# Optimization experiments

Measured on AMD Instinct MI355X. Metric: run time of the kernel, lower is better.

The kernel has to match this reference:

```python
import jax, jax.numpy as jnp
import numpy as np

NUM_LAYERS = 2
D = 1024
DIN = 2048
N_STATE = 16
K = 4
EPS = 1e-5


def layer_norm(x, w, b):
    m = jnp.mean(x, axis=-1, keepdims=True)
    v = jnp.mean(jnp.square(x - m), axis=-1, keepdims=True)
    return (x - m) * jax.lax.rsqrt(v + EPS) * w + b


def selective_ssm(x, A_log, Wdt, b_dt, WB, WC, D_skip):
    # x: [B, L, DIN]; diagonal selective SSM (Mamba-style)
    A = -jnp.exp(A_log)                      # [DIN, N]
    dt = jax.nn.softplus(x @ Wdt + b_dt)     # [B, L, DIN]
    Bm = x @ WB                              # [B, L, N]
    Cm = x @ WC                              # [B, L, N]

    def step(h, inp):
        x_t, dt_t, B_t, C_t = inp            # [B,DIN],[B,DIN],[B,N],[B,N]
        dA = jnp.exp(dt_t[..., None] * A)    # [B, DIN, N]
        h = h * dA + (dt_t * x_t)[..., None] * B_t[:, None, :]
        y = jnp.einsum('bdn,bn->bd', h, C_t)
        return h, y

    xs = (x.transpose(1, 0, 2), dt.transpose(1, 0, 2),
          Bm.transpose(1, 0, 2), Cm.transpose(1, 0, 2))
    h0 = jnp.zeros((x.shape[0], x.shape[2], N_STATE), x.dtype)
    h_last, ys = jax.lax.scan(step, h0, xs)
    y = ys.transpose(1, 0, 2) + x * D_skip
    return y, h_last


def causal_dwconv(x, w, b):
    # x: [B, L, DIN]; w: [K, DIN] depthwise causal conv
    xp = jnp.pad(x, ((0, 0), (K - 1, 0), (0, 0)))
    out = jax.lax.conv_general_dilated(
        xp, w[:, None, :], (1,), 'VALID',
        dimension_numbers=('NWC', 'WIO', 'NWC'),
        feature_group_count=x.shape[-1])
    return out + b


def setup_inputs() -> dict:
    key = jax.random.key(0)
    ks = jax.random.split(key, 12)
    s = 0.02
    B, L = 2, 2048
    return {
        'x': jax.random.normal(ks[0], (B, L, D), jnp.float32),
        'pos_emb': jax.random.normal(ks[1], (L, D), jnp.float32) * s,
        'norm_w': jnp.ones((NUM_LAYERS, D), jnp.float32),
        'norm_b': jnp.zeros((NUM_LAYERS, D), jnp.float32),
        'Win': jax.random.normal(ks[2], (NUM_LAYERS, D, DIN), jnp.float32) * s,
        'b_in': jnp.zeros((NUM_LAYERS, DIN), jnp.float32),
        'A_log': jax.random.uniform(ks[3], (NUM_LAYERS, DIN, N_STATE), jnp.float32),
        'Wdt': jax.random.normal(ks[4], (NUM_LAYERS, DIN, DIN), jnp.float32) * s,
        'b_dt': jax.random.normal(ks[5], (NUM_LAYERS, DIN), jnp.float32) - 4.0,
        'WB': jax.random.normal(ks[6], (NUM_LAYERS, DIN, N_STATE), jnp.float32) * s,
        'WC': jax.random.normal(ks[7], (NUM_LAYERS, DIN, N_STATE), jnp.float32) * s,
        'D_skip': jnp.ones((NUM_LAYERS, DIN), jnp.float32),
        'conv_w': jax.random.normal(ks[8], (NUM_LAYERS, K, DIN), jnp.float32) * s,
        'conv_b': jnp.zeros((NUM_LAYERS, DIN), jnp.float32),
        'Wout': jax.random.normal(ks[9], (NUM_LAYERS, DIN, D), jnp.float32) * s,
        'b_out': jnp.zeros((NUM_LAYERS, D), jnp.float32),
        'fnorm_w': jnp.ones((D,), jnp.float32),
        'fnorm_b': jnp.zeros((D,), jnp.float32),
    }


def reference(x, pos_emb, norm_w, norm_b, Win, b_in, A_log, Wdt, b_dt, WB, WC,
              D_skip, conv_w, conv_b, Wout, b_out, fnorm_w, fnorm_b):
    L = x.shape[1]
    x = x + pos_emb[:L]
    for i in range(NUM_LAYERS):
        res = x
        h = layer_norm(x, norm_w[i], norm_b[i])
        h = h @ Win[i] + b_in[i]                       # [B, L, DIN]
        y_ssm, _ = selective_ssm(h, A_log[i], Wdt[i], b_dt[i], WB[i], WC[i], D_skip[i])
        y_conv = jax.nn.silu(causal_dwconv(h, conv_w[i], conv_b[i]))
        g = y_ssm * jax.nn.sigmoid(y_conv)             # gating
        x = g @ Wout[i] + b_out[i] + res               # dropout is identity (eval)
    return layer_norm(x, fnorm_w, fnorm_b)
```

## Files before the change

### kernel.cpp

```cpp
#include <hip/hip_runtime.h>
#include <cstdint>
#include <cstddef>

#define D_MODEL 1024
#define DIN     2048
#define NSTATE  16
#define LSEQ    2048
#define NBATCH  2
#define NROWS   (NBATCH*LSEQ)
#define NCOL    (DIN + 128)
#define CCH     64
#define TC      (LSEQ/CCH)

typedef float  f32x4  __attribute__((ext_vector_type(4)));
typedef short  bf16x8 __attribute__((ext_vector_type(8)));
typedef unsigned short us8 __attribute__((ext_vector_type(8)));

__device__ __forceinline__ unsigned short f2bf(float f) {
  union { float f; unsigned u; } c; c.f = f;
  unsigned x = c.u + 0x7fffu + ((c.u >> 16) & 1u);
  return (unsigned short)(x >> 16);
}
__device__ __forceinline__ float bf2f(unsigned short u) {
  union { unsigned u; float f; } c; c.u = (unsigned)u << 16; return c.f;
}
__device__ __forceinline__ float sigmoidf_(float x) {
  return __builtin_amdgcn_rcpf(1.f + __expf(-x));
}
__device__ __forceinline__ float softplusf_(float x) {
  return fmaxf(x, 0.f) + __logf(1.f + __expf(-fabsf(x)));
}

__device__ __forceinline__ void gll16(const void* g, void* l) {
  __builtin_amdgcn_global_load_lds(
      (const __attribute__((address_space(1))) void*)g,
      (__attribute__((address_space(3))) void*)l, 16, 0, 0);
}

__global__ __launch_bounds__(256) void ln_kernel(const float* __restrict__ Xin,
    const float* __restrict__ pos, const unsigned short* __restrict__ P, int nP,
    const float* __restrict__ bex, const float* __restrict__ w,
    const float* __restrict__ b, unsigned short* __restrict__ outB,
    float* __restrict__ outF, float* __restrict__ Xw) {
  const int row = blockIdx.x, t = threadIdx.x;
  float4 v = *(const float4*)(Xin + (size_t)row * D_MODEL + t * 4);
  if (pos) {
    const float4 p = *(const float4*)(pos + (size_t)(row & (LSEQ - 1)) * D_MODEL + t * 4);
    v.x += p.x; v.y += p.y; v.z += p.z; v.w += p.w;
  }
  if (P) {
    const size_t MN = (size_t)NROWS * D_MODEL;
    const size_t e = (size_t)row * D_MODEL + t * 4;
    float a0 = 0.f, a1 = 0.f, a2 = 0.f, a3 = 0.f;
#pragma unroll 4
    for (int k = 0; k < nP; k++) {
      const ushort4 u = *(const ushort4*)(P + k * MN + e);
      a0 += bf2f(u.x); a1 += bf2f(u.y); a2 += bf2f(u.z); a3 += bf2f(u.w);
    }
    const float4 be = *(const float4*)(bex + t * 4);
    v.x += a0 + be.x; v.y += a1 + be.y; v.z += a2 + be.z; v.w += a3 + be.w;
  }
  if (Xw) *(float4*)(Xw + (size_t)row * D_MODEL + t * 4) = v;
  float s  = v.x + v.y + v.z + v.w;
  float s2 = v.x * v.x + v.y * v.y + v.z * v.z + v.w * v.w;
#pragma unroll
  for (int o = 1; o < 64; o <<= 1) { s += __shfl_xor(s, o, 64); s2 += __shfl_xor(s2, o, 64); }
  __shared__ float ps[8];
  int wv = t >> 6;
  if ((t & 63) == 0) { ps[wv] = s; ps[wv + 4] = s2; }
  __syncthreads();
  s  = ps[0] + ps[1] + ps[2] + ps[3];
  s2 = ps[4] + ps[5] + ps[6] + ps[7];
  float mean = s * (1.f / D_MODEL);
  float var  = s2 * (1.f / D_MODEL) - mean * mean;
  float rs   = rsqrtf(var + 1e-5f);
  const float4 wv4 = *(const float4*)(w + t * 4);
  const float4 bv4 = *(const float4*)(b + t * 4);
  float o0 = (v.x - mean) * rs * wv4.x + bv4.x;
  float o1 = (v.y - mean) * rs * wv4.y + bv4.y;
  float o2 = (v.z - mean) * rs * wv4.z + bv4.z;
  float o3 = (v.w - mean) * rs * wv4.w + bv4.w;
  if (outB) {
    ushort4 o; o.x = f2bf(o0); o.y = f2bf(o1); o.z = f2bf(o2); o.w = f2bf(o3);
    *(ushort4*)(outB + (size_t)row * D_MODEL + t * 4) = o;
  } else {
    float4 o; o.x = o0; o.y = o1; o.z = o2; o.w = o3;
    *(float4*)(outF + (size_t)row * D_MODEL + t * 4) = o;
  }
}

__global__ __launch_bounds__(256) void tcvt_kernel(const float* __restrict__ in0,
    unsigned short* __restrict__ out0, int K_, int N_,
    size_t inLS, size_t outLS) {
  const float* in = in0 + (size_t)blockIdx.z * inLS;
  unsigned short* out = out0 + (size_t)blockIdx.z * outLS;
  __shared__ float tile[64][68];
  int n0 = blockIdx.x * 64, k0 = blockIdx.y * 64;
  int t = threadIdx.x;
  int r = t >> 4, cc = (t & 15) * 4;
#pragma unroll
  for (int j = 0; j < 4; j++) {
    const float4 v = *(const float4*)(in + (size_t)(k0 + r + j * 16) * N_ + n0 + cc);
    tile[r + j * 16][cc + 0] = v.x; tile[r + j * 16][cc + 1] = v.y;
    tile[r + j * 16][cc + 2] = v.z; tile[r + j * 16][cc + 3] = v.w;
  }
  __syncthreads();
  int nr = t >> 2, kc = (t & 3) * 16;
  unsigned u[8];
#pragma unroll
  for (int i = 0; i < 8; i++) {
    unsigned lo = f2bf(tile[kc + 2 * i][nr]);
    unsigned hi = f2bf(tile[kc + 2 * i + 1][nr]);
    u[i] = lo | (hi << 16);
  }
  uint4* dst = (uint4*)(out + (size_t)(n0 + nr) * K_ + k0 + kc);
  uint4 w0; w0.x = u[0]; w0.y = u[1]; w0.z = u[2]; w0.w = u[3];
  uint4 w1; w1.x = u[4]; w1.y = u[5]; w1.z = u[6]; w1.w = u[7];
  dst[0] = w0; dst[1] = w1;
}

__global__ __launch_bounds__(256) void wprep_kernel(const float* __restrict__ WB0,
    const float* __restrict__ WC0, const float* __restrict__ b_dt0,
    unsigned short* __restrict__ Wt0, float* __restrict__ bias20) {
  const int L = blockIdx.y;
  const float* WB = WB0 + (size_t)L * DIN * NSTATE;
  const float* WC = WC0 + (size_t)L * DIN * NSTATE;
  const float* b_dt = b_dt0 + (size_t)L * DIN;
  unsigned short* Wt = Wt0 + (size_t)L * NCOL * DIN;
  float* bias2 = bias20 + (size_t)L * NCOL;
  int id = blockIdx.x * 256 + threadIdx.x;
  if (id < 65536) {
    int k = id & (DIN - 1);
    int n2 = id >> 11;
    float v = (n2 < NSTATE) ? WB[(size_t)k * NSTATE + n2]
                            : WC[(size_t)k * NSTATE + (n2 - NSTATE)];
    Wt[(size_t)(DIN + n2) * DIN + k] = f2bf(v);
  } else if (id < 90112) {
    int z = id - 65536;
    uint4 zz; zz.x = zz.y = zz.z = zz.w = 0u;
    *(uint4*)(Wt + (size_t)2080 * DIN + (size_t)z * 8) = zz;
  } else if (id < 90112 + NCOL) {
    int i = id - 90112;
    bias2[i] = (i < DIN) ? b_dt[i] : 0.f;
  }
}

__global__ __launch_bounds__(256) void gemm_kernel(
    const unsigned short* __restrict__ A, const unsigned short* __restrict__ Bt,
    const float* __restrict__ bias, unsigned short* __restrict__ outP,
    int M, int N, int Kfull, int kLen) {
  __shared__ unsigned short smem[6 * 128 * 32];
  unsigned short* sA = smem;
  unsigned short* sB = smem + 3 * 4096;
  const int t = threadIdx.x;
  const int lane = t & 63, wave = t >> 6;
  const int wr = wave >> 1, wc = wave & 1;

  const int gx = gridDim.x, gy = gridDim.y;
  const int orig = (blockIdx.z * gy + blockIdx.y) * gx + blockIdx.x;
  const int nwg = gx * gy * gridDim.z;
  const int q = nwg >> 3, r = nwg & 7;
  const int xcd = orig & 7, pp = orig >> 3;
  const int wgid = (xcd < r) ? (xcd * (q + 1) + pp)
                             : (r * (q + 1) + (xcd - r) * q + pp);
  const int nt = wgid % gx;
  const int mt = (wgid / gx) % gy;
  const int ks = wgid / (gx * gy);
  const int m0 = mt * 128, n0 = nt * 128;

  const int ar = t >> 2;
  const int acs = (((t & 3) ^ ((ar >> 1) & 3)) << 3);
  const int wseg = wave * 16 * 32;
  const int lr = lane & 15;
  const int swA = (((lane >> 4) ^ ((lr >> 1) & 3)) << 3);

  f32x4 acc[4][4];
#pragma unroll
  for (int m = 0; m < 4; m++)
#pragma unroll
    for (int n = 0; n < 4; n++) acc[m][n] = (f32x4)0.f;

  const int kBeg = ks * kLen;
  const int NT = kLen >> 5;

  auto STAGE = [&](int bi, int k0) {
    gll16(A  + (size_t)(m0 + ar) * Kfull + k0 + acs,      &sA[bi * 4096 + wseg]);
    gll16(A  + (size_t)(m0 + 64 + ar) * Kfull + k0 + acs, &sA[bi * 4096 + 64 * 32 + wseg]);
    gll16(Bt + (size_t)(n0 + ar) * Kfull + k0 + acs,      &sB[bi * 4096 + wseg]);
    gll16(Bt + (size_t)(n0 + 64 + ar) * Kfull + k0 + acs, &sB[bi * 4096 + 64 * 32 + wseg]);
  };
  auto COMPUTE = [&](int bi) {
    bf16x8 af[4], bg[4];
#pragma unroll
    for (int m = 0; m < 4; m++)
      af[m] = *(const bf16x8*)(&sA[bi * 4096 + (wr * 64 + m * 16 + lr) * 32 + swA]);
#pragma unroll
    for (int n = 0; n < 4; n++)
      bg[n] = *(const bf16x8*)(&sB[bi * 4096 + (wc * 64 + n * 16 + lr) * 32 + swA]);
#pragma unroll
    for (int m = 0; m < 4; m++)
#pragma unroll
      for (int n = 0; n < 4; n++)
        acc[m][n] = __builtin_amdgcn_mfma_f32_16x16x32_bf16(af[m], bg[n], acc[m][n], 0, 0, 0);
  };

  STAGE(0, kBeg); STAGE(1, kBeg + 32);
  for (int tt = 0; tt < NT - 1; ++tt) {
    asm volatile("s_waitcnt vmcnt(4)" ::: "memory");
    __builtin_amdgcn_s_barrier();
    if (tt + 2 < NT) STAGE((tt + 2) % 3, kBeg + ((tt + 2) << 5));
    COMPUTE(tt % 3);
  }
  asm volatile("s_waitcnt vmcnt(0)" ::: "memory");
  __builtin_amdgcn_s_barrier();
  COMPUTE((NT - 1) % 3);

  __syncthreads();
  unsigned short* sC = smem + wave * 4096;
  const int lq = lane >> 4;
#pragma unroll
  for (int m = 0; m < 4; m++)
#pragma unroll
    for (int n = 0; n < 4; n++) {
      const int lcol = n * 16 + lr;
      const float bv = (bias && ks == 0) ? bias[n0 + wc * 64 + lcol] : 0.f;
#pragma unroll
      for (int j = 0; j < 4; j++) {
        const int lrow = m * 16 + lq * 4 + j;
        const int sc = lcol ^ (((lrow >> 2) & 3) << 4);
        sC[lrow * 64 + sc] = f2bf(acc[m][n][j] + bv);
      }
    }
  unsigned short* out = outP + (size_t)ks * M * N;
  const int rowbase = m0 + wr * 64, colbase = n0 + wc * 64;
  const int rr = lane >> 3, ch = lane & 7;
#pragma unroll
  for (int i = 0; i < 8; i++) {
    const int row = i * 8 + rr;
    const int sb = (ch * 16) ^ (((row >> 2) & 3) << 5);
    us8 v = *(const us8*)((const char*)sC + row * 128 + sb);
    *(us8*)(out + (size_t)(rowbase + row) * N + colbase + ch * 8) = v;
  }
}

__global__ __launch_bounds__(256) void hfin_kernel(const unsigned short* __restrict__ P,
    const float* __restrict__ bias, unsigned short* __restrict__ Hbf) {
  const size_t e = ((size_t)blockIdx.x * 256 + threadIdx.x) * 4;
  const int col = (int)(e & (DIN - 1));
  const ushort4 u0 = *(const ushort4*)(P + e);
  const ushort4 u1 = *(const ushort4*)(P + (size_t)NROWS * DIN + e);
  const float4 b = *(const float4*)(bias + col);
  ushort4 o;
  o.x = f2bf(bf2f(u0.x) + bf2f(u1.x) + b.x);
  o.y = f2bf(bf2f(u0.y) + bf2f(u1.y) + b.y);
  o.z = f2bf(bf2f(u0.z) + bf2f(u1.z) + b.z);
  o.w = f2bf(bf2f(u0.w) + bf2f(u1.w) + b.w);
  *(ushort4*)(Hbf + e) = o;
}

__global__ __launch_bounds__(256) void scan1_kernel(
    const unsigned short* __restrict__ DTP, const unsigned short* __restrict__ Hbf,
    const float* __restrict__ A_log, float* __restrict__ Hc, float* __restrict__ Pc) {
  const unsigned short* DT1 = DTP + (size_t)NROWS * NCOL;
  const int tid = threadIdx.x;
  const int d0 = blockIdx.x * 256, d = d0 + tid;
  const int b = blockIdx.y, c = blockIdx.z;
  __shared__ unsigned short ssp[TC][256];
  __shared__ unsigned short sxx[TC][256];
  __shared__ float sBC[TC][32];
  const size_t base = (size_t)b * LSEQ + c * TC;
#pragma unroll
  for (int it = 0; it < TC * 32 / 256; ++it) {
    int idx = it * 256 + tid;
    int tt = idx >> 5, cc = (idx & 31) * 8;
    us8 a = *(const us8*)(DTP + (base + tt) * NCOL + d0 + cc);
    us8 bb = *(const us8*)(DT1 + (base + tt) * NCOL + d0 + cc);
    us8 o;
#pragma unroll
    for (int j = 0; j < 8; j++) o[j] = f2bf(softplusf_(bf2f(a[j]) + bf2f(bb[j])));
    *(us8*)&ssp[tt][cc] = o;
    *(us8*)&sxx[tt][cc] = *(const us8*)(Hbf + (base + tt) * DIN + d0 + cc);
  }
  if (tid < TC * 4) {
    int tt = tid >> 2, cc = (tid & 3) * 8;
    us8 v0 = *(const us8*)(DTP + (base + tt) * NCOL + DIN + cc);
    us8 v1 = *(const us8*)(DT1 + (base + tt) * NCOL + DIN + cc);
#pragma unroll
    for (int j = 0; j < 8; j++) sBC[tt][cc + j] = bf2f(v0[j]) + bf2f(v1[j]);
  }
  float a2[16], h[16];
#pragma unroll
  for (int n = 0; n < 16; n++) {
    a2[n] = -__expf(A_log[(size_t)d * NSTATE + n]);
    h[n] = 0.f;
  }
  __syncthreads();
  float S = 0.f;
  for (int tt = 0; tt < TC; ++tt) {
    float sp = bf2f(ssp[tt][tid]);
    float x  = bf2f(sxx[tt][tid]);
    S += sp;
    float sx = sp * x;
#pragma unroll
    for (int n = 0; n < 16; n++)
      h[n] = fmaf(h[n], __expf(sp * a2[n]), sx * sBC[tt][n]);
  }
  const size_t chain = ((size_t)c * (NBATCH * DIN) + (size_t)b * DIN + d) * 16;
#pragma unroll
  for (int n = 0; n < 16; n++) {
    Hc[chain + n] = h[n];
    Pc[chain + n] = __expf(S * a2[n]);
  }
}

__global__ __launch_bounds__(256) void scomb_kernel(float* __restrict__ Hc,
    const float* __restrict__ Pc) {
  const size_t id = (size_t)blockIdx.x * 256 + threadIdx.x;
  const size_t stride = (size_t)NBATCH * DIN * NSTATE;
  float h = 0.f;
  for (int c = 0; c < CCH; c++) {
    size_t o = (size_t)c * stride + id;
    float hl = Hc[o], p = Pc[o];
    Hc[o] = h;
    h = fmaf(p, h, hl);
  }
}

__global__ __launch_bounds__(256) void scan2g_kernel(
    const unsigned short* __restrict__ DTP, const unsigned short* __restrict__ Hbf,
    const float* __restrict__ A_log, const float* __restrict__ Hinit,
    const float* __restrict__ cw, const float* __restrict__ cb,
    const float* __restrict__ dsk, unsigned short* __restrict__ G) {
  const unsigned short* DT1 = DTP + (size_t)NROWS * NCOL;
  const int tid = threadIdx.x;
  const int d0 = blockIdx.x * 256, d = d0 + tid;
  const int b = blockIdx.y, c = blockIdx.z;
  __shared__ unsigned short ssp[TC][256];
  __shared__ unsigned short sxx[TC][256];
  __shared__ float sBC[TC][32];
  const size_t base = (size_t)b * LSEQ + c * TC;
#pragma unroll
  for (int it = 0; it < TC * 32 / 256; ++it) {
    int idx = it * 256 + tid;
    int tt = idx >> 5, cc = (idx & 31) * 8;
    us8 a = *(const us8*)(DTP + (base + tt) * NCOL + d0 + cc);
    us8 bb = *(const us8*)(DT1 + (base + tt) * NCOL + d0 + cc);
    us8 o;
#pragma unroll
    for (int j = 0; j < 8; j++) o[j] = f2bf(softplusf_(bf2f(a[j]) + bf2f(bb[j])));
    *(us8*)&ssp[tt][cc] = o;
    *(us8*)&sxx[tt][cc] = *(const us8*)(Hbf + (base + tt) * DIN + d0 + cc);
  }
  if (tid < TC * 4) {
    int tt = tid >> 2, cc = (tid & 3) * 8;
    us8 v0 = *(const us8*)(DTP + (base + tt) * NCOL + DIN + cc);
    us8 v1 = *(const us8*)(DT1 + (base + tt) * NCOL + DIN + cc);
#pragma unroll
    for (int j = 0; j < 8; j++) sBC[tt][cc + j] = bf2f(v0[j]) + bf2f(v1[j]);
  }
  const size_t chain = ((size_t)c * (NBATCH * DIN) + (size_t)b * DIN + d) * 16;
  float a2[16], h[16];
#pragma unroll
  for (int n = 0; n < 16; n++) {
    a2[n] = -__expf(A_log[(size_t)d * NSTATE + n]);
    h[n] = Hinit[chain + n];
  }
  const float w0 = cw[d], w1 = cw[DIN + d], w2 = cw[2 * DIN + d], w3 = cw[3 * DIN + d];
  const float cbv = cb[d], dsv = dsk[d];
  const int t0 = c * TC;
  float xm1 = (t0 >= 1) ? bf2f(Hbf[(base - 1) * DIN + d]) : 0.f;
  float xm2 = (t0 >= 2) ? bf2f(Hbf[(base - 2) * DIN + d]) : 0.f;
  float xm3 = (t0 >= 3) ? bf2f(Hbf[(base - 3) * DIN + d]) : 0.f;
  __syncthreads();
  for (int tt = 0; tt < TC; ++tt) {
    float sp = bf2f(ssp[tt][tid]);
    float x  = bf2f(sxx[tt][tid]);
    float sx = sp * x;
    float y0 = 0.f, y1 = 0.f, y2 = 0.f, y3 = 0.f;
#pragma unroll
    for (int n = 0; n < 16; n += 4) {
      h[n]     = fmaf(h[n],     __expf(sp * a2[n]),     sx * sBC[tt][n]);
      h[n + 1] = fmaf(h[n + 1], __expf(sp * a2[n + 1]), sx * sBC[tt][n + 1]);
      h[n + 2] = fmaf(h[n + 2], __expf(sp * a2[n + 2]), sx * sBC[tt][n + 2]);
      h[n + 3] = fmaf(h[n + 3], __expf(sp * a2[n + 3]), sx * sBC[tt][n + 3]);
      y0 = fmaf(h[n],     sBC[tt][16 + n],     y0);
      y1 = fmaf(h[n + 1], sBC[tt][16 + n + 1], y1);
      y2 = fmaf(h[n + 2], sBC[tt][16 + n + 2], y2);
      y3 = fmaf(h[n + 3], sBC[tt][16 + n + 3], y3);
    }
    float y = (y0 + y1) + (y2 + y3);
    float a = cbv + w0 * xm3 + w1 * xm2 + w2 * xm1 + w3 * x;
    float sl = a * sigmoidf_(a);
    float g = (y + x * dsv) * sigmoidf_(sl);
    G[(base + tt) * DIN + d] = f2bf(g);
    xm3 = xm2; xm2 = xm1; xm1 = x;
  }
}

extern "C" void kernel_launch(void* const* d_in, const int* in_sizes, int n_in,
                              void* d_out, int out_size, void* d_ws, size_t ws_size,
                              hipStream_t stream) {
  const float* x_in   = (const float*)d_in[0];
  const float* pos    = (const float*)d_in[1];
  const float* norm_w = (const float*)d_in[2];
  const float* norm_b = (const float*)d_in[3];
  const float* Win    = (const float*)d_in[4];
  const float* b_in   = (const float*)d_in[5];
  const float* A_log  = (const float*)d_in[6];
  const float* Wdt    = (const float*)d_in[7];
  const float* b_dt   = (const float*)d_in[8];
  const float* WB     = (const float*)d_in[9];
  const float* WC     = (const float*)d_in[10];
  const float* Dsk    = (const float*)d_in[11];
  const float* conv_w = (const float*)d_in[12];
  const float* conv_b = (const float*)d_in[13];
  const float* Wout   = (const float*)d_in[14];
  const float* b_out  = (const float*)d_in[15];
  const float* fnw    = (const float*)d_in[16];
  const float* fnb    = (const float*)d_in[17];

  uint8_t* ws = (uint8_t*)d_ws;
  constexpr size_t OFF_X     = 0;
  constexpr size_t OFF_HBF   = 16777216;
  constexpr size_t OFF_DT    = 33554432;
  constexpr size_t OFF_XG    = 69206016;
  constexpr size_t OFF_HC    = 85983232;
  constexpr size_t OFF_PC    = 102760448;
  constexpr size_t OFF_WINT  = 119537664;
  constexpr size_t OFF_WDT   = 127926272;
  constexpr size_t OFF_WOUT  = 145752064;
  constexpr size_t OFF_BIAS2 = 154140672;
  constexpr size_t WS_NEEDED = 154158080;
  if (ws_size < WS_NEEDED) return;

  float* X             = (float*)(ws + OFF_X);
  unsigned short* Hbf  = (unsigned short*)(ws + OFF_HBF);
  unsigned short* DTP  = (unsigned short*)(ws + OFF_DT);
  unsigned short* Xn   = (unsigned short*)(ws + OFF_XG);
  unsigned short* Gb   = (unsigned short*)(ws + OFF_XG);
  float* Hc            = (float*)(ws + OFF_HC);
  float* Pc            = (float*)(ws + OFF_PC);
  unsigned short* WinT   = (unsigned short*)(ws + OFF_WINT);
  unsigned short* WdtBCT = (unsigned short*)(ws + OFF_WDT);
  unsigned short* WoutT  = (unsigned short*)(ws + OFF_WOUT);
  float* bias2         = (float*)(ws + OFF_BIAS2);

  tcvt_kernel<<<dim3(32, 16, 2), 256, 0, stream>>>(
      Win, WinT, 1024, 2048, (size_t)D_MODEL * DIN, (size_t)DIN * D_MODEL);
  tcvt_kernel<<<dim3(32, 32, 2), 256, 0, stream>>>(
      Wdt, WdtBCT, 2048, 2048, (size_t)DIN * DIN, (size_t)NCOL * DIN);
  tcvt_kernel<<<dim3(16, 32, 2), 256, 0, stream>>>(
      Wout, WoutT, 2048, 1024, (size_t)DIN * D_MODEL, (size_t)D_MODEL * DIN);
  wprep_kernel<<<dim3(361, 2), 256, 0, stream>>>(WB, WC, b_dt, WdtBCT, bias2);

  for (int i = 0; i < 2; i++) {
    unsigned short* WinT_i   = WinT + (size_t)i * DIN * D_MODEL;
    unsigned short* WdtBCT_i = WdtBCT + (size_t)i * NCOL * DIN;
    unsigned short* WoutT_i  = WoutT + (size_t)i * D_MODEL * DIN;
    float* bias2_i           = bias2 + (size_t)i * NCOL;

    if (i == 0)
      ln_kernel<<<4096, 256, 0, stream>>>(x_in, pos, nullptr, 0, nullptr,
                                          norm_w, norm_b, Xn, nullptr, X);
    else
      ln_kernel<<<4096, 256, 0, stream>>>(X, nullptr, DTP, 4, b_out,
                                          norm_w + D_MODEL, norm_b + D_MODEL,
                                          Xn, nullptr, X);
    gemm_kernel<<<dim3(16, 32, 2), 256, 0, stream>>>(
        Xn, WinT_i, nullptr, DTP, NROWS, DIN, D_MODEL, 512);
    hfin_kernel<<<8192, 256, 0, stream>>>(DTP, b_in + (size_t)i * DIN, Hbf);
    gemm_kernel<<<dim3(17, 32, 2), 256, 0, stream>>>(
        Hbf, WdtBCT_i, bias2_i, DTP, NROWS, NCOL, DIN, 1024);
    scan1_kernel<<<dim3(DIN / 256, NBATCH, CCH), 256, 0, stream>>>(
        DTP, Hbf, A_log + (size_t)i * DIN * NSTATE, Hc, Pc);
    scomb_kernel<<<(NBATCH * DIN * NSTATE) / 256, 256, 0, stream>>>(Hc, Pc);
    scan2g_kernel<<<dim3(DIN / 256, NBATCH, CCH), 256, 0, stream>>>(
        DTP, Hbf, A_log + (size_t)i * DIN * NSTATE, Hc,
        conv_w + (size_t)i * 4 * DIN, conv_b + (size_t)i * DIN,
        Dsk + (size_t)i * DIN, Gb);
    gemm_kernel<<<dim3(8, 32, 4), 256, 0, stream>>>(
        Gb, WoutT_i, nullptr, DTP, NROWS, D_MODEL, DIN, 512);
  }

  ln_kernel<<<4096, 256, 0, stream>>>(X, nullptr, DTP, 4, b_out + D_MODEL,
                                      fnw, fnb, nullptr, (float*)d_out, nullptr);
}
```

Measured before the change: 465.9 us.

## Drop split-K on Win/Wdt GEMMs, fuse bias and softplus into epilogue

The Win and Wdt/B/C GEMMs no longer use split-K. Bias, and softplus for the dt columns, are now applied in the GEMM epilogue. This removes the hfin reduction kernel and the per-scan-kernel summing of two partial buffers and softplus recomputation. The Wout GEMM split-K drops from 4 to 2, so the layer-norm kernels reduce fewer partials. The cost is fewer workgroups per GEMM (512 and 544 tiles, 512 for Wout) and longer K loops per tile, which may lower occupancy across the CUs.

```diff
diff --git a/kernel.cpp b/kernel.cpp
--- a/kernel.cpp
+++ b/kernel.cpp
@@ -52,7 +52,7 @@
     const size_t MN = (size_t)NROWS * D_MODEL;
     const size_t e = (size_t)row * D_MODEL + t * 4;
     float a0 = 0.f, a1 = 0.f, a2 = 0.f, a3 = 0.f;
-#pragma unroll 4
+#pragma unroll 2
     for (int k = 0; k < nP; k++) {
       const ushort4 u = *(const ushort4*)(P + k * MN + e);
       a0 += bf2f(u.x); a1 += bf2f(u.y); a2 += bf2f(u.z); a3 += bf2f(u.w);
@@ -148,7 +148,7 @@
 __global__ __launch_bounds__(256) void gemm_kernel(
     const unsigned short* __restrict__ A, const unsigned short* __restrict__ Bt,
     const float* __restrict__ bias, unsigned short* __restrict__ outP,
-    int M, int N, int Kfull, int kLen) {
+    int M, int N, int Kfull, int kLen, int spCols) {
   __shared__ unsigned short smem[6 * 128 * 32];
   unsigned short* sA = smem;
   unsigned short* sB = smem + 3 * 4096;
@@ -223,12 +223,16 @@
 #pragma unroll
     for (int n = 0; n < 4; n++) {
       const int lcol = n * 16 + lr;
-      const float bv = (bias && ks == 0) ? bias[n0 + wc * 64 + lcol] : 0.f;
+      const int col = n0 + wc * 64 + lcol;
+      const float bv = (bias && ks == 0) ? bias[col] : 0.f;
+      const bool sp = col < spCols;
 #pragma unroll
       for (int j = 0; j < 4; j++) {
         const int lrow = m * 16 + lq * 4 + j;
         const int sc = lcol ^ (((lrow >> 2) & 3) << 4);
-        sC[lrow * 64 + sc] = f2bf(acc[m][n][j] + bv);
+        float v = acc[m][n][j] + bv;
+        if (sp) v = softplusf_(v);
+        sC[lrow * 64 + sc] = f2bf(v);
       }
     }
   unsigned short* out = outP + (size_t)ks * M * N;
@@ -243,25 +247,9 @@
   }
 }
 
-__global__ __launch_bounds__(256) void hfin_kernel(const unsigned short* __restrict__ P,
-    const float* __restrict__ bias, unsigned short* __restrict__ Hbf) {
-  const size_t e = ((size_t)blockIdx.x * 256 + threadIdx.x) * 4;
-  const int col = (int)(e & (DIN - 1));
-  const ushort4 u0 = *(const ushort4*)(P + e);
-  const ushort4 u1 = *(const ushort4*)(P + (size_t)NROWS * DIN + e);
-  const float4 b = *(const float4*)(bias + col);
-  ushort4 o;
-  o.x = f2bf(bf2f(u0.x) + bf2f(u1.x) + b.x);
-  o.y = f2bf(bf2f(u0.y) + bf2f(u1.y) + b.y);
-  o.z = f2bf(bf2f(u0.z) + bf2f(u1.z) + b.z);
-  o.w = f2bf(bf2f(u0.w) + bf2f(u1.w) + b.w);
-  *(ushort4*)(Hbf + e) = o;
-}
-
 __global__ __launch_bounds__(256) void scan1_kernel(
-    const unsigned short* __restrict__ DTP, const unsigned short* __restrict__ Hbf,
+    const unsigned short* __restrict__ DTF, const unsigned short* __restrict__ Hbf,
     const float* __restrict__ A_log, float* __restrict__ Hc, float* __restrict__ Pc) {
-  const unsigned short* DT1 = DTP + (size_t)NROWS * NCOL;
   const int tid = threadIdx.x;
   const int d0 = blockIdx.x * 256, d = d0 + tid;
   const int b = blockIdx.y, c = blockIdx.z;
@@ -273,20 +261,14 @@
   for (int it = 0; it < TC * 32 / 256; ++it) {
     int idx = it * 256 + tid;
     int tt = idx >> 5, cc = (idx & 31) * 8;
-    us8 a = *(const us8*)(DTP + (base + tt) * NCOL + d0 + cc);
-    us8 bb = *(const us8*)(DT1 + (base + tt) * NCOL + d0 + cc);
-    us8 o;
-#pragma unroll
-    for (int j = 0; j < 8; j++) o[j] = f2bf(softplusf_(bf2f(a[j]) + bf2f(bb[j])));
-    *(us8*)&ssp[tt][cc] = o;
+    *(us8*)&ssp[tt][cc] = *(const us8*)(DTF + (base + tt) * NCOL + d0 + cc);
     *(us8*)&sxx[tt][cc] = *(const us8*)(Hbf + (base + tt) * DIN + d0 + cc);
   }
   if (tid < TC * 4) {
     int tt = tid >> 2, cc = (tid & 3) * 8;
-    us8 v0 = *(const us8*)(DTP + (base + tt) * NCOL + DIN + cc);
-    us8 v1 = *(const us8*)(DT1 + (base + tt) * NCOL + DIN + cc);
-#pragma unroll
-    for (int j = 0; j < 8; j++) sBC[tt][cc + j] = bf2f(v0[j]) + bf2f(v1[j]);
+    us8 v = *(const us8*)(DTF + (base + tt) * NCOL + DIN + cc);
+#pragma unroll
+    for (int j = 0; j < 8; j++) sBC[tt][cc + j] = bf2f(v[j]);
   }
   float a2[16], h[16];
 #pragma unroll
@@ -327,11 +309,10 @@
 }
 
 __global__ __launch_bounds__(256) void scan2g_kernel(
-    const unsigned short* __restrict__ DTP, const unsigned short* __restrict__ Hbf,
+    const unsigned short* __restrict__ DTF, const unsigned short* __restrict__ Hbf,
     const float* __restrict__ A_log, const float* __restrict__ Hinit,
     const float* __restrict__ cw, const float* __restrict__ cb,
     const float* __restrict__ dsk, unsigned short* __restrict__ G) {
-  const unsigned short* DT1 = DTP + (size_t)NROWS * NCOL;
   const int tid = threadIdx.x;
   const int d0 = blockIdx.x * 256, d = d0 + tid;
   const int b = blockIdx.y, c = blockIdx.z;
@@ -343,20 +324,14 @@
   for (int it = 0; it < TC * 32 / 256; ++it) {
     int idx = it * 256 + tid;
     int tt = idx >> 5, cc = (idx & 31) * 8;
-    us8 a = *(const us8*)(DTP + (base + tt) * NCOL + d0 + cc);
-    us8 bb = *(const us8*)(DT1 + (base + tt) * NCOL + d0 + cc);
-    us8 o;
-#pragma unroll
-    for (int j = 0; j < 8; j++) o[j] = f2bf(softplusf_(bf2f(a[j]) + bf2f(bb[j])));
-    *(us8*)&ssp[tt][cc] = o;
+    *(us8*)&ssp[tt][cc] = *(const us8*)(DTF + (base + tt) * NCOL + d0 + cc);
     *(us8*)&sxx[tt][cc] = *(const us8*)(Hbf + (base + tt) * DIN + d0 + cc);
   }
   if (tid < TC * 4) {
     int tt = tid >> 2, cc = (tid & 3) * 8;
-    us8 v0 = *(const us8*)(DTP + (base + tt) * NCOL + DIN + cc);
-    us8 v1 = *(const us8*)(DT1 + (base + tt) * NCOL + DIN + cc);
-#pragma unroll
-    for (int j = 0; j < 8; j++) sBC[tt][cc + j] = bf2f(v0[j]) + bf2f(v1[j]);
+    us8 v = *(const us8*)(DTF + (base + tt) * NCOL + DIN + cc);
+#pragma unroll
+    for (int j = 0; j < 8; j++) sBC[tt][cc + j] = bf2f(v[j]);
   }
   const size_t chain = ((size_t)c * (NBATCH * DIN) + (size_t)b * DIN + d) * 16;
   float a2[16], h[16];
@@ -435,7 +410,8 @@
 
   float* X             = (float*)(ws + OFF_X);
   unsigned short* Hbf  = (unsigned short*)(ws + OFF_HBF);
-  unsigned short* DTP  = (unsigned short*)(ws + OFF_DT);
+  unsigned short* DTF  = (unsigned short*)(ws + OFF_DT);
+  unsigned short* WoutP= (unsigned short*)(ws + OFF_DT);
   unsigned short* Xn   = (unsigned short*)(ws + OFF_XG);
   unsigned short* Gb   = (unsigned short*)(ws + OFF_XG);
   float* Hc            = (float*)(ws + OFF_HC);
@@ -463,25 +439,24 @@
       ln_kernel<<<4096, 256, 0, stream>>>(x_in, pos, nullptr, 0, nullptr,
                                           norm_w, norm_b, Xn, nullptr, X);
     else
-      ln_kernel<<<4096, 256, 0, stream>>>(X, nullptr, DTP, 4, b_out,
+      ln_kernel<<<4096, 256, 0, stream>>>(X, nullptr, WoutP, 2, b_out,
                                           norm_w + D_MODEL, norm_b + D_MODEL,
                                           Xn, nullptr, X);
-    gemm_kernel<<<dim3(16, 32, 2), 256, 0, stream>>>(
-        Xn, WinT_i, nullptr, DTP, NROWS, DIN, D_MODEL, 512);
-    hfin_kernel<<<8192, 256, 0, stream>>>(DTP, b_in + (size_t)i * DIN, Hbf);
-    gemm_kernel<<<dim3(17, 32, 2), 256, 0, stream>>>(
-        Hbf, WdtBCT_i, bias2_i, DTP, NROWS, NCOL, DIN, 1024);
+    gemm_kernel<<<dim3(16, 32, 1), 256, 0, stream>>>(
+        Xn, WinT_i, b_in + (size_t)i * DIN, Hbf, NROWS, DIN, D_MODEL, 1024, 0);
+    gemm_kernel<<<dim3(17, 32, 1), 256, 0, stream>>>(
+        Hbf, WdtBCT_i, bias2_i, DTF, NROWS, NCOL, DIN, 2048, DIN);
     scan1_kernel<<<dim3(DIN / 256, NBATCH, CCH), 256, 0, stream>>>(
-        DTP, Hbf, A_log + (size_t)i * DIN * NSTATE, Hc, Pc);
+        DTF, Hbf, A_log + (size_t)i * DIN * NSTATE, Hc, Pc);
     scomb_kernel<<<(NBATCH * DIN * NSTATE) / 256, 256, 0, stream>>>(Hc, Pc);
     scan2g_kernel<<<dim3(DIN / 256, NBATCH, CCH), 256, 0, stream>>>(
-        DTP, Hbf, A_log + (size_t)i * DIN * NSTATE, Hc,
+        DTF, Hbf, A_log + (size_t)i * DIN * NSTATE, Hc,
         conv_w + (size_t)i * 4 * DIN, conv_b + (size_t)i * DIN,
         Dsk + (size_t)i * DIN, Gb);
-    gemm_kernel<<<dim3(8, 32, 4), 256, 0, stream>>>(
-        Gb, WoutT_i, nullptr, DTP, NROWS, D_MODEL, DIN, 512);
-  }
-
-  ln_kernel<<<4096, 256, 0, stream>>>(X, nullptr, DTP, 4, b_out + D_MODEL,
+    gemm_kernel<<<dim3(8, 32, 2), 256, 0, stream>>>(
+        Gb, WoutT_i, nullptr, WoutP, NROWS, D_MODEL, DIN, 1024, 0);
+  }
+
+  ln_kernel<<<4096, 256, 0, stream>>>(X, nullptr, WoutP, 2, b_out + D_MODEL,
                                       fnw, fnb, nullptr, (float*)d_out, nullptr);
 }
```

Result: faster. 449.7 us (-3.5%).
